# Performance work log

Hardware: AMD Instinct MI355X
Metric: run time of the kernel (lower is better)

The kernel has to match this reference:

```python
import jax, jax.numpy as jnp
import numpy as np

N_HEAD = 16
LORA_SCALE = 1.0 / 4.0  # alpha=1, r=4
LN_EPS = 1e-5


def _ln(x, g, b):
    # LayerNorm subclass casts to float32 then back to input dtype
    xf = x.astype(jnp.float32)
    m = xf.mean(-1, keepdims=True)
    v = xf.var(-1, keepdims=True)
    y = (xf - m) / jnp.sqrt(v + LN_EPS) * g + b
    return y.astype(x.dtype)


def _lora(h, a, b):
    # x @ a.T @ b.T * scaling ; a:[r,d], b:[d,r]
    return (h @ a.T) @ b.T * LORA_SCALE


def _attn(h, Wq, bq, Wk, Wv, bv, Wo, bo, la_k, lb_k, la_v, lb_v, la_o, lb_o):
    B, S, D = h.shape
    hd = D // N_HEAD
    scale = hd ** (-0.25)
    q = h @ Wq.T + bq
    k = h @ Wk.T + _lora(h, la_k, lb_k)          # key Linear has no bias
    v = h @ Wv.T + bv + _lora(h, la_v, lb_v)
    qh = q.reshape(B, S, N_HEAD, hd).transpose(0, 2, 1, 3) * scale  # [B,H,S,hd]
    kh = k.reshape(B, S, N_HEAD, hd).transpose(0, 2, 1, 3) * scale
    vh = v.reshape(B, S, N_HEAD, hd).transpose(0, 2, 1, 3)
    qk = jnp.einsum('bhqd,bhkd->bhqk', qh, kh).astype(jnp.float32)
    w = jax.nn.softmax(qk, axis=-1).astype(q.dtype)
    wv = jnp.einsum('bhqk,bhkd->bhqd', w, vh)
    wv = wv.transpose(0, 2, 1, 3).reshape(B, S, D)
    return wv @ Wo.T + bo + _lora(wv, la_o, lb_o)


def setup_inputs() -> dict:
    key = jax.random.key(0)
    D, R = 1024, 4
    B, S = 8, 1024
    ks = jax.random.split(key, 20)
    sd = 0.02
    inp = {
        'x': jax.random.normal(ks[0], (B, S, D), jnp.float32),
        'Wq': jax.random.normal(ks[1], (D, D), jnp.float32) * sd,
        'bq': jnp.zeros((D,), jnp.float32),
        'Wk': jax.random.normal(ks[2], (D, D), jnp.float32) * sd,
        'Wv': jax.random.normal(ks[3], (D, D), jnp.float32) * sd,
        'bv': jnp.zeros((D,), jnp.float32),
        'Wo': jax.random.normal(ks[4], (D, D), jnp.float32) * sd,
        'bo': jnp.zeros((D,), jnp.float32),
        'la_k': jax.random.normal(ks[5], (R, D), jnp.float32) * sd,
        'lb_k': jax.random.normal(ks[6], (D, R), jnp.float32) * sd,
        'la_v': jax.random.normal(ks[7], (R, D), jnp.float32) * sd,
        'lb_v': jax.random.normal(ks[8], (D, R), jnp.float32) * sd,
        'la_o': jax.random.normal(ks[9], (R, D), jnp.float32) * sd,
        'lb_o': jax.random.normal(ks[10], (D, R), jnp.float32) * sd,
        'g_attn': jnp.ones((D,), jnp.float32),
        'b_attn': jnp.zeros((D,), jnp.float32),
        'W1': jax.random.normal(ks[11], (4 * D, D), jnp.float32) * sd,
        'b1': jnp.zeros((4 * D,), jnp.float32),
        'W2': jax.random.normal(ks[12], (D, 4 * D), jnp.float32) * sd,
        'b2': jnp.zeros((D,), jnp.float32),
        'g_mlp': jnp.ones((D,), jnp.float32),
        'b_mlp': jnp.zeros((D,), jnp.float32),
    }
    return inp


def reference(x, Wq, bq, Wk, Wv, bv, Wo, bo, la_k, lb_k, la_v, lb_v, la_o, lb_o,
              g_attn, b_attn, W1, b1, W2, b2, g_mlp, b_mlp):
    # self-attention + residual (LoRA on key/value/out)
    x = x + _attn(_ln(x, g_attn, b_attn), Wq, bq, Wk, Wv, bv, Wo, bo,
                  la_k, lb_k, la_v, lb_v, la_o, lb_o)
    # MLP + residual (exact GELU, matching nn.GELU default)
    h = _ln(x, g_mlp, b_mlp)
    h = jax.nn.gelu(h @ W1.T + b1, approximate=False)
    x = x + h @ W2.T + b2
    return x
```

## Files before the change

kernel.cpp:

```cpp
#include <hip/hip_runtime.h>
#include <math.h>

typedef _Float16 f16_t;
typedef f16_t f16x8 __attribute__((ext_vector_type(8)));
typedef f16_t f16x4 __attribute__((ext_vector_type(4)));
typedef float f32x4 __attribute__((ext_vector_type(4)));
typedef float fv4 __attribute__((ext_vector_type(4)));

#define MFMA16(a, b, c) __builtin_amdgcn_mfma_f32_16x16x32_f16(a, b, c, 0, 0, 0)

__device__ __forceinline__ void gload16(const void* g, void* l) {
  __builtin_amdgcn_global_load_lds((const __attribute__((address_space(1))) void*)g,
                                   (__attribute__((address_space(3))) void*)l, 16, 0, 0);
}

__global__ __launch_bounds__(256) void ln_f32(const float* __restrict__ x,
                                              const float* __restrict__ g,
                                              const float* __restrict__ b,
                                              f16_t* __restrict__ y) {
  const int D = 1024;
  int row = blockIdx.x;
  int t = threadIdx.x;
  const float* xr = x + (size_t)row * D + t * 4;
  float x0 = xr[0], x1 = xr[1], x2 = xr[2], x3 = xr[3];
  float sum = x0 + x1 + x2 + x3;
  float sq = x0 * x0 + x1 * x1 + x2 * x2 + x3 * x3;
  for (int d = 32; d; d >>= 1) {
    sum += __shfl_down(sum, d);
    sq += __shfl_down(sq, d);
  }
  __shared__ float ssum[4], ssq[4];
  int w = t >> 6, lane = t & 63;
  if (lane == 0) { ssum[w] = sum; ssq[w] = sq; }
  __syncthreads();
  float ts = ssum[0] + ssum[1] + ssum[2] + ssum[3];
  float tq = ssq[0] + ssq[1] + ssq[2] + ssq[3];
  float mean = ts * (1.0f / 1024.0f);
  float var = tq * (1.0f / 1024.0f) - mean * mean;
  float rstd = rsqrtf(var + 1e-5f);
  f16_t* yr = y + (size_t)row * D + t * 4;
  const float* gr = g + t * 4;
  const float* br = b + t * 4;
  yr[0] = (f16_t)((x0 - mean) * rstd * gr[0] + br[0]);
  yr[1] = (f16_t)((x1 - mean) * rstd * gr[1] + br[1]);
  yr[2] = (f16_t)((x2 - mean) * rstd * gr[2] + br[2]);
  yr[3] = (f16_t)((x3 - mean) * rstd * gr[3] + br[3]);
}

__global__ __launch_bounds__(256) void ln_f16(const f16_t* __restrict__ x,
                                              const float* __restrict__ g,
                                              const float* __restrict__ b,
                                              f16_t* __restrict__ y) {
  const int D = 1024;
  int row = blockIdx.x;
  int t = threadIdx.x;
  const f16_t* xr = x + (size_t)row * D + t * 4;
  float x0 = (float)xr[0], x1 = (float)xr[1], x2 = (float)xr[2], x3 = (float)xr[3];
  float sum = x0 + x1 + x2 + x3;
  float sq = x0 * x0 + x1 * x1 + x2 * x2 + x3 * x3;
  for (int d = 32; d; d >>= 1) {
    sum += __shfl_down(sum, d);
    sq += __shfl_down(sq, d);
  }
  __shared__ float ssum[4], ssq[4];
  int w = t >> 6, lane = t & 63;
  if (lane == 0) { ssum[w] = sum; ssq[w] = sq; }
  __syncthreads();
  float ts = ssum[0] + ssum[1] + ssum[2] + ssum[3];
  float tq = ssq[0] + ssq[1] + ssq[2] + ssq[3];
  float mean = ts * (1.0f / 1024.0f);
  float var = tq * (1.0f / 1024.0f) - mean * mean;
  float rstd = rsqrtf(var + 1e-5f);
  f16_t* yr = y + (size_t)row * D + t * 4;
  const float* gr = g + t * 4;
  const float* br = b + t * 4;
  yr[0] = (f16_t)((x0 - mean) * rstd * gr[0] + br[0]);
  yr[1] = (f16_t)((x1 - mean) * rstd * gr[1] + br[1]);
  yr[2] = (f16_t)((x2 - mean) * rstd * gr[2] + br[2]);
  yr[3] = (f16_t)((x3 - mean) * rstd * gr[3] + br[3]);
}

__global__ __launch_bounds__(256) void convert_w(
    const float* __restrict__ wq, const float* __restrict__ wk,
    const float* __restrict__ wv, const float* __restrict__ wo,
    const float* __restrict__ w1, const float* __restrict__ w2,
    f16_t* __restrict__ oq, f16_t* __restrict__ ok, f16_t* __restrict__ ov,
    f16_t* __restrict__ oo, f16_t* __restrict__ o1, f16_t* __restrict__ o2) {
  int bid = blockIdx.x;
  const float* src;
  f16_t* dst;
  int bi;
  if (bid < 2048) {
    int seg = bid >> 9;
    bi = bid & 511;
    src = seg == 0 ? wq : seg == 1 ? wk : seg == 2 ? wv : wo;
    dst = seg == 0 ? oq : seg == 1 ? ok : seg == 2 ? ov : oo;
  } else if (bid < 4096) {
    bi = bid - 2048; src = w1; dst = o1;
  } else {
    bi = bid - 4096; src = w2; dst = o2;
  }
  size_t idx = (size_t)bi * 2048 + (size_t)threadIdx.x * 8;
  fv4 a = *(const fv4*)(src + idx);
  fv4 b = *(const fv4*)(src + idx + 4);
  f16x8 h;
#pragma unroll
  for (int j = 0; j < 4; ++j) { h[j] = (f16_t)a[j]; h[4 + j] = (f16_t)b[j]; }
  *(f16x8*)(dst + idx) = h;
}

__global__ __launch_bounds__(256) void lora_t_kernel(const f16_t* __restrict__ h,
                                                     const float* __restrict__ la,
                                                     float* __restrict__ t, int K) {
  int lane = threadIdx.x & 63;
  int w = threadIdx.x >> 6;
  int row = blockIdx.x * 4 + w;
  const f16_t* hrow = h + (size_t)row * K;
  float acc[4] = {0.f, 0.f, 0.f, 0.f};
  for (int it = 0; it < K / 512; ++it) {
    int base = it * 512 + lane * 8;
    f16x8 hx = *(const f16x8*)(hrow + base);
#pragma unroll
    for (int r = 0; r < 4; ++r) {
      const float* ar = la + (size_t)r * K + base;
#pragma unroll
      for (int j = 0; j < 8; ++j) acc[r] += (float)hx[j] * ar[j];
    }
  }
#pragma unroll
  for (int r = 0; r < 4; ++r) {
    for (int d = 32; d; d >>= 1) acc[r] += __shfl_down(acc[r], d);
  }
  if (lane == 0) {
#pragma unroll
    for (int r = 0; r < 4; ++r) t[(size_t)row * 4 + r] = acc[r];
  }
}

__global__ __launch_bounds__(256, 2) void gemm_f16(
    const f16_t* __restrict__ A, const f16_t* __restrict__ B,
    const float* __restrict__ bias, const float* __restrict__ loraT,
    const float* __restrict__ loraB, const float* residf,
    const f16_t* __restrict__ residb, f16_t* Cb, float* Cf, f16_t* Cvt,
    int M, int N, int K, int ldb, int dogelu) {
  __shared__ __align__(16) f16_t smem[2][16384];
  const int tid = threadIdx.x;
  const int lane = tid & 63, wid = tid >> 6;
  const int wm = wid >> 1, wn = wid & 1;
  const int l15 = lane & 15, lhi = lane >> 4;
  int nwg = gridDim.x * gridDim.y;
  int bid = blockIdx.y * gridDim.x + blockIdx.x;
  int swz = (bid & 7) * (nwg >> 3) + (bid >> 3);
  const int m0 = (swz / gridDim.x) * 128, n0 = (swz % gridDim.x) * 128;
  const int arow = tid >> 3;
  const int aslot = tid & 7;

  f32x4 acc[4][4];
#pragma unroll
  for (int i = 0; i < 4; ++i)
#pragma unroll
    for (int j = 0; j < 4; ++j) acc[i][j] = (f32x4){0.f, 0.f, 0.f, 0.f};

  auto stage = [&](const f16_t* G, int r0, int ldg, int step, char* lds) {
#pragma unroll
    for (int c = 0; c < 4; ++c) {
      int r = c * 32 + arow;
      int cm = aslot ^ (r & 7);
      gload16(G + (size_t)(r0 + r) * ldg + (size_t)step * 64 + cm * 8,
              lds + c * 4096 + wid * 1024);
    }
  };

  const int nsteps = K >> 6;
  stage(A, m0, K, 0, (char*)&smem[0][0]);
  stage(B, n0, ldb, 0, (char*)&smem[0][8192]);
  __syncthreads();
  for (int t = 0; t < nsteps; ++t) {
    int cur = t & 1, nxt = cur ^ 1;
    if (t + 1 < nsteps) {
      stage(A, m0, K, t + 1, (char*)&smem[nxt][0]);
      stage(B, n0, ldb, t + 1, (char*)&smem[nxt][8192]);
    }
    const char* As = (const char*)&smem[cur][0];
    const char* Bs = (const char*)&smem[cur][8192];
#pragma unroll
    for (int kk = 0; kk < 2; ++kk) {
      f16x8 af[4], bf[4];
#pragma unroll
      for (int i = 0; i < 4; ++i) {
        int row = wm * 64 + i * 16 + l15;
        af[i] = *(const f16x8*)(As + row * 128 + ((kk * 64 + lhi * 16) ^ ((row & 7) << 4)));
      }
#pragma unroll
      for (int j = 0; j < 4; ++j) {
        int row = wn * 64 + j * 16 + l15;
        bf[j] = *(const f16x8*)(Bs + row * 128 + ((kk * 64 + lhi * 16) ^ ((row & 7) << 4)));
      }
#pragma unroll
      for (int i = 0; i < 4; ++i)
#pragma unroll
        for (int j = 0; j < 4; ++j) acc[i][j] = MFMA16(af[i], bf[j], acc[i][j]);
    }
    __syncthreads();
  }

  const int gm = m0 + wm * 64, gn = n0 + wn * 64;
#pragma unroll
  for (int j = 0; j < 4; ++j) {
    int gcol = gn + j * 16 + l15;
    float bj = bias ? bias[gcol] : 0.f;
    float lb0 = 0.f, lb1 = 0.f, lb2 = 0.f, lb3 = 0.f;
    if (loraB) {
      const float* p = loraB + (size_t)gcol * 4;
      lb0 = p[0]; lb1 = p[1]; lb2 = p[2]; lb3 = p[3];
    }
#pragma unroll
    for (int i = 0; i < 4; ++i) {
      float v4[4];
#pragma unroll
      for (int r = 0; r < 4; ++r) {
        int grow = gm + i * 16 + lhi * 4 + r;
        float val = acc[i][j][r] + bj;
        if (loraT) {
          const float* tp = loraT + (size_t)grow * 4;
          val += 0.25f * (tp[0] * lb0 + tp[1] * lb1 + tp[2] * lb2 + tp[3] * lb3);
        }
        if (dogelu) val = 0.5f * val * (1.0f + erff(val * 0.70710678118654752f));
        if (residf) val += residf[(size_t)grow * N + gcol];
        if (residb) val += (float)residb[(size_t)grow * N + gcol];
        v4[r] = val;
      }
      if (Cf) {
#pragma unroll
        for (int r = 0; r < 4; ++r)
          Cf[(size_t)(gm + i * 16 + lhi * 4 + r) * N + gcol] = v4[r];
      } else if (Cvt) {
        int grow0 = gm + i * 16 + lhi * 4;
        int bb = grow0 >> 10, ss = grow0 & 1023;
        int hh = gcol >> 6, dd = gcol & 63;
        f16x4 pk;
#pragma unroll
        for (int r = 0; r < 4; ++r) pk[r] = (f16_t)v4[r];
        *(f16x4*)(Cvt + (((size_t)bb * 16 + hh) * 64 + dd) * 1024 + ss) = pk;
      } else {
#pragma unroll
        for (int r = 0; r < 4; ++r)
          Cb[(size_t)(gm + i * 16 + lhi * 4 + r) * N + gcol] = (f16_t)v4[r];
      }
    }
  }
}

__global__ __launch_bounds__(256, 2) void gemm_mfma(
    const f16_t* __restrict__ A, const float* __restrict__ B,
    const float* __restrict__ bias, const float* __restrict__ loraT,
    const float* __restrict__ loraB, const float* residf,
    const f16_t* __restrict__ residb, f16_t* Cb, float* Cf, f16_t* Cvt,
    int M, int N, int K, int ldb, int dogelu) {
  __shared__ __align__(16) f16_t smem[2][16384];
  const int tid = threadIdx.x;
  const int lane = tid & 63, wid = tid >> 6;
  const int wm = wid >> 1, wn = wid & 1;
  const int l15 = lane & 15, lhi = lane >> 4;
  const int m0 = blockIdx.y * 128, n0 = blockIdx.x * 128;
  const int arow = tid >> 3;
  const int aslot = tid & 7;

  f32x4 acc[4][4];
#pragma unroll
  for (int i = 0; i < 4; ++i)
#pragma unroll
    for (int j = 0; j < 4; ++j) acc[i][j] = (f32x4){0.f, 0.f, 0.f, 0.f};

  fv4 breg[4][2];

  auto stageA = [&](int step, int buf) {
#pragma unroll
    for (int c = 0; c < 4; ++c) {
      int r = c * 32 + arow;
      int cm = aslot ^ (r & 7);
      gload16(A + (size_t)(m0 + r) * K + (size_t)step * 64 + cm * 8,
              (char*)&smem[buf][0] + c * 4096 + wid * 1024);
    }
  };
  auto loadB = [&](int step) {
#pragma unroll
    for (int c = 0; c < 4; ++c) {
      int r = c * 32 + arow;
      const float* gp = B + (size_t)(n0 + r) * ldb + (size_t)step * 64 + aslot * 8;
      breg[c][0] = *(const fv4*)gp;
      breg[c][1] = *(const fv4*)(gp + 4);
    }
  };
  auto writeB = [&](int buf) {
#pragma unroll
    for (int c = 0; c < 4; ++c) {
      int r = c * 32 + arow;
      f16x8 hh;
#pragma unroll
      for (int j = 0; j < 4; ++j) hh[j] = (f16_t)breg[c][0][j];
#pragma unroll
      for (int j = 0; j < 4; ++j) hh[4 + j] = (f16_t)breg[c][1][j];
      int boff = r * 128 + ((aslot * 16) ^ ((r & 7) << 4));
      *(f16x8*)((char*)&smem[buf][8192] + boff) = hh;
    }
  };

  const int nsteps = K >> 6;
  stageA(0, 0);
  loadB(0);
  writeB(0);
  __syncthreads();
  for (int t = 0; t < nsteps; ++t) {
    int cur = t & 1, nxt = cur ^ 1;
    if (t + 1 < nsteps) { stageA(t + 1, nxt); loadB(t + 1); }
    const char* As = (const char*)&smem[cur][0];
    const char* Bs = (const char*)&smem[cur][8192];
#pragma unroll
    for (int kk = 0; kk < 2; ++kk) {
      f16x8 af[4], bf[4];
#pragma unroll
      for (int i = 0; i < 4; ++i) {
        int row = wm * 64 + i * 16 + l15;
        af[i] = *(const f16x8*)(As + row * 128 + ((kk * 64 + lhi * 16) ^ ((row & 7) << 4)));
      }
#pragma unroll
      for (int j = 0; j < 4; ++j) {
        int row = wn * 64 + j * 16 + l15;
        bf[j] = *(const f16x8*)(Bs + row * 128 + ((kk * 64 + lhi * 16) ^ ((row & 7) << 4)));
      }
#pragma unroll
      for (int i = 0; i < 4; ++i)
#pragma unroll
        for (int j = 0; j < 4; ++j) acc[i][j] = MFMA16(af[i], bf[j], acc[i][j]);
    }
    if (t + 1 < nsteps) writeB(nxt);
    __syncthreads();
  }

  const int gm = m0 + wm * 64, gn = n0 + wn * 64;
#pragma unroll
  for (int j = 0; j < 4; ++j) {
    int gcol = gn + j * 16 + l15;
    float bj = bias ? bias[gcol] : 0.f;
    float lb0 = 0.f, lb1 = 0.f, lb2 = 0.f, lb3 = 0.f;
    if (loraB) {
      const float* p = loraB + (size_t)gcol * 4;
      lb0 = p[0]; lb1 = p[1]; lb2 = p[2]; lb3 = p[3];
    }
#pragma unroll
    for (int i = 0; i < 4; ++i) {
      float v4[4];
#pragma unroll
      for (int r = 0; r < 4; ++r) {
        int grow = gm + i * 16 + lhi * 4 + r;
        float val = acc[i][j][r] + bj;
        if (loraT) {
          const float* tp = loraT + (size_t)grow * 4;
          val += 0.25f * (tp[0] * lb0 + tp[1] * lb1 + tp[2] * lb2 + tp[3] * lb3);
        }
        if (dogelu) val = 0.5f * val * (1.0f + erff(val * 0.70710678118654752f));
        if (residf) val += residf[(size_t)grow * N + gcol];
        if (residb) val += (float)residb[(size_t)grow * N + gcol];
        v4[r] = val;
      }
      if (Cf) {
#pragma unroll
        for (int r = 0; r < 4; ++r)
          Cf[(size_t)(gm + i * 16 + lhi * 4 + r) * N + gcol] = v4[r];
      } else if (Cvt) {
        int grow0 = gm + i * 16 + lhi * 4;
        int bb = grow0 >> 10, ss = grow0 & 1023;
        int hh = gcol >> 6, dd = gcol & 63;
        f16x4 pk;
#pragma unroll
        for (int r = 0; r < 4; ++r) pk[r] = (f16_t)v4[r];
        *(f16x4*)(Cvt + (((size_t)bb * 16 + hh) * 64 + dd) * 1024 + ss) = pk;
      } else {
#pragma unroll
        for (int r = 0; r < 4; ++r)
          Cb[(size_t)(gm + i * 16 + lhi * 4 + r) * N + gcol] = (f16_t)v4[r];
      }
    }
  }
}

__global__ __launch_bounds__(256, 3) void attn_mfma(const f16_t* __restrict__ q,
                                                    const f16_t* __restrict__ k,
                                                    const f16_t* __restrict__ vt,
                                                    f16_t* __restrict__ wv) {
  const int S = 1024, D = 1024;
  __shared__ __align__(16) f16_t Qs[128 * 64];
  __shared__ __align__(16) f16_t SP[128 * 64];
  __shared__ __align__(16) f16_t Ks[64 * 64];
  __shared__ __align__(16) f16_t Vts[64 * 64];
  __shared__ float rsb[128];
  __shared__ float lib[128];
  const int tid = threadIdx.x, lane = tid & 63, w = tid >> 6;
  const int l15 = lane & 15, lhi = lane >> 4;
  const int q0 = blockIdx.x * 128;
  const int h = blockIdx.y, b = blockIdx.z;
  const f16_t* qg = q + ((size_t)b * S + q0) * D + h * 64;
  const f16_t* kg = k + (size_t)b * S * D + h * 64;
  const f16_t* vg = vt + ((size_t)b * 16 + h) * 64 * (size_t)S;

#pragma unroll
  for (int c = 0; c < 4; ++c) {
    int r = c * 32 + (tid >> 3), kc = tid & 7;
    f16x8 xx = *(const f16x8*)(qg + (size_t)r * D + kc * 8);
    *(f16x8*)((char*)Qs + r * 128 + ((kc * 16) ^ ((r & 7) << 4))) = xx;
  }
  __syncthreads();
  f16x8 qf[2][2];
#pragma unroll
  for (int i = 0; i < 2; ++i) {
    int row = w * 32 + i * 16 + l15;
#pragma unroll
    for (int kk = 0; kk < 2; ++kk)
      qf[i][kk] = *(const f16x8*)((char*)Qs + row * 128 +
                                  ((kk * 64 + lhi * 16) ^ ((row & 7) << 4)));
  }

  f32x4 oacc[2][4];
#pragma unroll
  for (int i = 0; i < 2; ++i)
#pragma unroll
    for (int j = 0; j < 4; ++j) oacc[i][j] = (f32x4){0.f, 0.f, 0.f, 0.f};
  float m_run = -1e30f, l_run = 0.f;
  const int myrow = w * 32 + (lane >> 1);
  const int half = lane & 1;

  for (int kv = 0; kv < 16; ++kv) {
    __syncthreads();
#pragma unroll
    for (int c = 0; c < 2; ++c) {
      int r = c * 32 + (tid >> 3), kc = tid & 7;
      f16x8 xk = *(const f16x8*)(kg + (size_t)(kv * 64 + r) * D + kc * 8);
      *(f16x8*)((char*)Ks + r * 128 + ((kc * 16) ^ ((r & 7) << 4))) = xk;
      f16x8 xv = *(const f16x8*)(vg + (size_t)r * S + kv * 64 + kc * 8);
      *(f16x8*)((char*)Vts + r * 128 + ((kc * 16) ^ ((r & 7) << 4))) = xv;
    }
    __syncthreads();
    f32x4 sacc[2][4];
#pragma unroll
    for (int i = 0; i < 2; ++i)
#pragma unroll
      for (int j = 0; j < 4; ++j) sacc[i][j] = (f32x4){0.f, 0.f, 0.f, 0.f};
#pragma unroll
    for (int kk = 0; kk < 2; ++kk) {
      f16x8 kf[4];
#pragma unroll
      for (int j = 0; j < 4; ++j) {
        int row = j * 16 + l15;
        kf[j] = *(const f16x8*)((char*)Ks + row * 128 +
                                ((kk * 64 + lhi * 16) ^ ((row & 7) << 4)));
      }
#pragma unroll
      for (int i = 0; i < 2; ++i)
#pragma unroll
        for (int j = 0; j < 4; ++j) sacc[i][j] = MFMA16(qf[i][kk], kf[j], sacc[i][j]);
    }
#pragma unroll
    for (int i = 0; i < 2; ++i)
#pragma unroll
      for (int j = 0; j < 4; ++j)
#pragma unroll
        for (int r = 0; r < 4; ++r) {
          int srow = w * 32 + i * 16 + lhi * 4 + r;
          int scol = j * 16 + l15;
          *(f16_t*)((char*)SP + srow * 128 + ((scol * 2) ^ ((srow & 7) << 4))) =
              (f16_t)(sacc[i][j][r] * 0.125f);
        }
    __syncthreads();
    f16x8 ch[4];
#pragma unroll
    for (int c = 0; c < 4; ++c)
      ch[c] = *(const f16x8*)((char*)SP + myrow * 128 +
                              ((half * 64 + c * 16) ^ ((myrow & 7) << 4)));
    float mt = -1e30f;
#pragma unroll
    for (int c = 0; c < 4; ++c)
#pragma unroll
      for (int e = 0; e < 8; ++e) mt = fmaxf(mt, (float)ch[c][e]);
    mt = fmaxf(mt, __shfl_xor(mt, 1));
    float mnew = fmaxf(m_run, mt);
    float resc = __expf(m_run - mnew);
    float lsum = 0.f;
#pragma unroll
    for (int c = 0; c < 4; ++c) {
      f16x8 p8;
#pragma unroll
      for (int e = 0; e < 8; ++e) {
        float p = __expf((float)ch[c][e] - mnew);
        lsum += p;
        p8[e] = (f16_t)p;
      }
      *(f16x8*)((char*)SP + myrow * 128 + ((half * 64 + c * 16) ^ ((myrow & 7) << 4))) = p8;
    }
    lsum += __shfl_xor(lsum, 1);
    l_run = l_run * resc + lsum;
    m_run = mnew;
    if (half == 0) rsb[myrow] = resc;
    __syncthreads();
#pragma unroll
    for (int i = 0; i < 2; ++i) {
      float f0 = rsb[w * 32 + i * 16 + lhi * 4 + 0];
      float f1 = rsb[w * 32 + i * 16 + lhi * 4 + 1];
      float f2 = rsb[w * 32 + i * 16 + lhi * 4 + 2];
      float f3 = rsb[w * 32 + i * 16 + lhi * 4 + 3];
#pragma unroll
      for (int j = 0; j < 4; ++j) {
        oacc[i][j][0] *= f0;
        oacc[i][j][1] *= f1;
        oacc[i][j][2] *= f2;
        oacc[i][j][3] *= f3;
      }
    }
#pragma unroll
    for (int kk = 0; kk < 2; ++kk) {
      f16x8 pa[2], vb[4];
#pragma unroll
      for (int i = 0; i < 2; ++i) {
        int row = w * 32 + i * 16 + l15;
        pa[i] = *(const f16x8*)((char*)SP + row * 128 +
                                ((kk * 64 + lhi * 16) ^ ((row & 7) << 4)));
      }
#pragma unroll
      for (int j = 0; j < 4; ++j) {
        int row = j * 16 + l15;
        vb[j] = *(const f16x8*)((char*)Vts + row * 128 +
                                ((kk * 64 + lhi * 16) ^ ((row & 7) << 4)));
      }
#pragma unroll
      for (int i = 0; i < 2; ++i)
#pragma unroll
        for (int j = 0; j < 4; ++j) oacc[i][j] = MFMA16(pa[i], vb[j], oacc[i][j]);
    }
  }
  if (half == 0) lib[myrow] = 1.f / l_run;
  __syncthreads();
#pragma unroll
  for (int i = 0; i < 2; ++i)
#pragma unroll
    for (int r = 0; r < 4; ++r) {
      int row = w * 32 + i * 16 + lhi * 4 + r;
      float li = lib[row];
      size_t base = ((size_t)b * S + q0 + row) * D + h * 64;
#pragma unroll
      for (int j = 0; j < 4; ++j)
        wv[base + j * 16 + l15] = (f16_t)(oacc[i][j][r] * li);
    }
}

extern "C" void kernel_launch(void* const* d_in, const int* in_sizes, int n_in,
                              void* d_out, int out_size, void* d_ws, size_t ws_size,
                              hipStream_t stream) {
  const int B = 8, S = 1024, D = 1024, F = 4096;
  const int M = B * S;

  const float* x = (const float*)d_in[0];
  const float* Wq = (const float*)d_in[1];
  const float* bq = (const float*)d_in[2];
  const float* Wk = (const float*)d_in[3];
  const float* Wv = (const float*)d_in[4];
  const float* bv = (const float*)d_in[5];
  const float* Wo = (const float*)d_in[6];
  const float* bo = (const float*)d_in[7];
  const float* la_k = (const float*)d_in[8];
  const float* lb_k = (const float*)d_in[9];
  const float* la_v = (const float*)d_in[10];
  const float* lb_v = (const float*)d_in[11];
  const float* la_o = (const float*)d_in[12];
  const float* lb_o = (const float*)d_in[13];
  const float* g_attn = (const float*)d_in[14];
  const float* b_attn = (const float*)d_in[15];
  const float* W1 = (const float*)d_in[16];
  const float* b1 = (const float*)d_in[17];
  const float* W2 = (const float*)d_in[18];
  const float* b2 = (const float*)d_in[19];
  const float* g_mlp = (const float*)d_in[20];
  const float* b_mlp = (const float*)d_in[21];

  float* t_k = (float*)((char*)d_ws + 16);
  float* t_v = t_k + (size_t)M * 4;
  float* t_o = t_v + (size_t)M * 4;
  const size_t MD = (size_t)M * D;
  f16_t* P0 = (f16_t*)((char*)d_ws + 409600);
  f16_t* P1 = P0 + MD;
  f16_t* P2 = P0 + 2 * MD;
  f16_t* P3 = P0 + 3 * MD;
  f16_t* Wqf = P0 + 4 * MD;
  f16_t* Wkf = Wqf + (size_t)D * D;
  f16_t* Wvf = Wkf + (size_t)D * D;
  f16_t* Wof = Wvf + (size_t)D * D;
  f16_t* W1f = Wof + (size_t)D * D;
  f16_t* W2f = W1f + (size_t)F * D;
  float* outf = (float*)d_out;
  const size_t need = 409600 + 4 * MD * sizeof(f16_t) +
                      (4 * (size_t)D * D + 2 * (size_t)F * D) * sizeof(f16_t);
  const bool f16w = ws_size >= need;

  if (f16w)
    convert_w<<<6144, 256, 0, stream>>>(Wq, Wk, Wv, Wo, W1, W2,
                                        Wqf, Wkf, Wvf, Wof, W1f, W2f);

  ln_f32<<<M, 256, 0, stream>>>(x, g_attn, b_attn, P0);
  lora_t_kernel<<<M / 4, 256, 0, stream>>>(P0, la_k, t_k, D);
  lora_t_kernel<<<M / 4, 256, 0, stream>>>(P0, la_v, t_v, D);
  if (f16w) {
    gemm_f16<<<dim3(8, 64), 256, 0, stream>>>(
        P0, Wqf, bq, nullptr, nullptr, nullptr, nullptr, P1, nullptr, nullptr,
        M, D, D, D, 0);
    gemm_f16<<<dim3(8, 64), 256, 0, stream>>>(
        P0, Wkf, nullptr, t_k, lb_k, nullptr, nullptr, P2, nullptr, nullptr,
        M, D, D, D, 0);
    gemm_f16<<<dim3(8, 64), 256, 0, stream>>>(
        P0, Wvf, bv, t_v, lb_v, nullptr, nullptr, nullptr, nullptr, P3,
        M, D, D, D, 0);
  } else {
    gemm_mfma<<<dim3(8, 64), 256, 0, stream>>>(
        P0, Wq, bq, nullptr, nullptr, nullptr, nullptr, P1, nullptr, nullptr,
        M, D, D, D, 0);
    gemm_mfma<<<dim3(8, 64), 256, 0, stream>>>(
        P0, Wk, nullptr, t_k, lb_k, nullptr, nullptr, P2, nullptr, nullptr,
        M, D, D, D, 0);
    gemm_mfma<<<dim3(8, 64), 256, 0, stream>>>(
        P0, Wv, bv, t_v, lb_v, nullptr, nullptr, nullptr, nullptr, P3,
        M, D, D, D, 0);
  }
  attn_mfma<<<dim3(8, 16, 8), 256, 0, stream>>>(P1, P2, P3, P0);
  lora_t_kernel<<<M / 4, 256, 0, stream>>>(P0, la_o, t_o, D);
  if (f16w)
    gemm_f16<<<dim3(8, 64), 256, 0, stream>>>(
        P0, Wof, bo, t_o, lb_o, x, nullptr, P3, nullptr, nullptr, M, D, D, D, 0);
  else
    gemm_mfma<<<dim3(8, 64), 256, 0, stream>>>(
        P0, Wo, bo, t_o, lb_o, x, nullptr, P3, nullptr, nullptr, M, D, D, D, 0);
  ln_f16<<<M, 256, 0, stream>>>(P3, g_mlp, b_mlp, P0);
  if (f16w) {
    gemm_f16<<<dim3(16, 64), 256, 0, stream>>>(
        P0, W1f, b1, nullptr, nullptr, nullptr, nullptr, P1, nullptr, nullptr,
        M, 2048, D, D, 1);
    gemm_f16<<<dim3(8, 64), 256, 0, stream>>>(
        P1, W2f, b2, nullptr, nullptr, nullptr, P3, nullptr, outf, nullptr,
        M, D, 2048, F, 0);
    gemm_f16<<<dim3(16, 64), 256, 0, stream>>>(
        P0, W1f + (size_t)2048 * D, b1 + 2048, nullptr, nullptr, nullptr, nullptr,
        P1, nullptr, nullptr, M, 2048, D, D, 1);
    gemm_f16<<<dim3(8, 64), 256, 0, stream>>>(
        P1, W2f + 2048, nullptr, nullptr, nullptr, outf, nullptr, nullptr, outf,
        nullptr, M, D, 2048, F, 0);
  } else {
    gemm_mfma<<<dim3(16, 64), 256, 0, stream>>>(
        P0, W1, b1, nullptr, nullptr, nullptr, nullptr, P1, nullptr, nullptr,
        M, 2048, D, D, 1);
    gemm_mfma<<<dim3(8, 64), 256, 0, stream>>>(
        P1, W2, b2, nullptr, nullptr, nullptr, P3, nullptr, outf, nullptr,
        M, D, 2048, F, 0);
    gemm_mfma<<<dim3(16, 64), 256, 0, stream>>>(
        P0, W1 + (size_t)2048 * D, b1 + 2048, nullptr, nullptr, nullptr, nullptr,
        P1, nullptr, nullptr, M, 2048, D, D, 1);
    gemm_mfma<<<dim3(8, 64), 256, 0, stream>>>(
        P1, W2 + 2048, nullptr, nullptr, nullptr, outf, nullptr, nullptr, outf,
        nullptr, M, D, 2048, F, 0);
  }
}
```

Measured before the change: 662.5 us.

## Fuse QKV projections into one GEMM and merge K/V LoRA kernels

Stores the Wq/Wk/Wv f16 copies contiguously so a single gemm_qkv launch over a 3072-wide N covers all three projections, with a per-segment epilogue for bias, LoRA and the transposed V layout. The two LoRA-A reductions for K and V become one kernel that reads the LN output once. Both GEMMs drop LDS double buffering for a single buffer and raise the occupancy hint to 3 blocks per CU, trading load/compute overlap within a block for more resident blocks to hide latency.

```diff
diff --git a/kernel.cpp b/kernel.cpp
--- a/kernel.cpp
+++ b/kernel.cpp
@@ -109,6 +109,47 @@
   *(f16x8*)(dst + idx) = h;
 }
 
+__global__ __launch_bounds__(256) void lora_kv_kernel(
+    const f16_t* __restrict__ h, const float* __restrict__ la_k,
+    const float* __restrict__ la_v, float* __restrict__ t_k,
+    float* __restrict__ t_v, int K) {
+  int lane = threadIdx.x & 63;
+  int w = threadIdx.x >> 6;
+  int row = blockIdx.x * 4 + w;
+  const f16_t* hrow = h + (size_t)row * K;
+  float ak[4] = {0.f, 0.f, 0.f, 0.f};
+  float av[4] = {0.f, 0.f, 0.f, 0.f};
+  for (int it = 0; it < K / 512; ++it) {
+    int base = it * 512 + lane * 8;
+    f16x8 hx = *(const f16x8*)(hrow + base);
+#pragma unroll
+    for (int r = 0; r < 4; ++r) {
+      const float* kr = la_k + (size_t)r * K + base;
+      const float* vr = la_v + (size_t)r * K + base;
+#pragma unroll
+      for (int j = 0; j < 8; ++j) {
+        float hv = (float)hx[j];
+        ak[r] += hv * kr[j];
+        av[r] += hv * vr[j];
+      }
+    }
+  }
+#pragma unroll
+  for (int r = 0; r < 4; ++r) {
+    for (int d = 32; d; d >>= 1) {
+      ak[r] += __shfl_down(ak[r], d);
+      av[r] += __shfl_down(av[r], d);
+    }
+  }
+  if (lane == 0) {
+#pragma unroll
+    for (int r = 0; r < 4; ++r) {
+      t_k[(size_t)row * 4 + r] = ak[r];
+      t_v[(size_t)row * 4 + r] = av[r];
+    }
+  }
+}
+
 __global__ __launch_bounds__(256) void lora_t_kernel(const f16_t* __restrict__ h,
                                                      const float* __restrict__ la,
                                                      float* __restrict__ t, int K) {
@@ -137,13 +178,123 @@
   }
 }
 
-__global__ __launch_bounds__(256, 2) void gemm_f16(
+__global__ __launch_bounds__(256, 3) void gemm_qkv(
+    const f16_t* __restrict__ A, const f16_t* __restrict__ W,
+    const float* __restrict__ bq, const float* __restrict__ bv,
+    const float* __restrict__ t_k, const float* __restrict__ lb_k,
+    const float* __restrict__ t_v, const float* __restrict__ lb_v,
+    f16_t* __restrict__ Pq, f16_t* __restrict__ Pk, f16_t* __restrict__ Pvt,
+    int K) {
+  const int D = 1024;
+  __shared__ __align__(16) f16_t Asm[8192];
+  __shared__ __align__(16) f16_t Bsm[8192];
+  const int tid = threadIdx.x;
+  const int lane = tid & 63, wid = tid >> 6;
+  const int wm = wid >> 1, wn = wid & 1;
+  const int l15 = lane & 15, lhi = lane >> 4;
+  int nwg = gridDim.x * gridDim.y;
+  int bid = blockIdx.y * gridDim.x + blockIdx.x;
+  int swz = (bid & 7) * (nwg >> 3) + (bid >> 3);
+  const int m0 = (swz / gridDim.x) * 128, n0 = (swz % gridDim.x) * 128;
+  const int seg = n0 >> 10;
+  const int arow = tid >> 3;
+  const int aslot = tid & 7;
+
+  f32x4 acc[4][4];
+#pragma unroll
+  for (int i = 0; i < 4; ++i)
+#pragma unroll
+    for (int j = 0; j < 4; ++j) acc[i][j] = (f32x4){0.f, 0.f, 0.f, 0.f};
+
+  auto stage = [&](const f16_t* G, int r0, int ldg, int step, char* lds) {
+#pragma unroll
+    for (int c = 0; c < 4; ++c) {
+      int r = c * 32 + arow;
+      int cm = aslot ^ (r & 7);
+      gload16(G + (size_t)(r0 + r) * ldg + (size_t)step * 64 + cm * 8,
+              lds + c * 4096 + wid * 1024);
+    }
+  };
+
+  const int nsteps = K >> 6;
+  for (int t = 0; t < nsteps; ++t) {
+    if (t) __syncthreads();
+    stage(A, m0, K, t, (char*)Asm);
+    stage(W, n0, K, t, (char*)Bsm);
+    __syncthreads();
+#pragma unroll
+    for (int kk = 0; kk < 2; ++kk) {
+      f16x8 af[4], bf[4];
+#pragma unroll
+      for (int i = 0; i < 4; ++i) {
+        int row = wm * 64 + i * 16 + l15;
+        af[i] = *(const f16x8*)((char*)Asm + row * 128 +
+                                ((kk * 64 + lhi * 16) ^ ((row & 7) << 4)));
+      }
+#pragma unroll
+      for (int j = 0; j < 4; ++j) {
+        int row = wn * 64 + j * 16 + l15;
+        bf[j] = *(const f16x8*)((char*)Bsm + row * 128 +
+                                ((kk * 64 + lhi * 16) ^ ((row & 7) << 4)));
+      }
+#pragma unroll
+      for (int i = 0; i < 4; ++i)
+#pragma unroll
+        for (int j = 0; j < 4; ++j) acc[i][j] = MFMA16(af[i], bf[j], acc[i][j]);
+    }
+  }
+
+  const int gm = m0 + wm * 64, gn = n0 + wn * 64;
+  const float* tB = (seg == 1) ? t_k : t_v;
+#pragma unroll
+  for (int j = 0; j < 4; ++j) {
+    int gcol = gn + j * 16 + l15;
+    int c = gcol & 1023;
+    float bj = (seg == 0) ? bq[c] : (seg == 2 ? bv[c] : 0.f);
+    float lb0 = 0.f, lb1 = 0.f, lb2 = 0.f, lb3 = 0.f;
+    if (seg) {
+      const float* p = (seg == 1 ? lb_k : lb_v) + (size_t)c * 4;
+      lb0 = p[0]; lb1 = p[1]; lb2 = p[2]; lb3 = p[3];
+    }
+#pragma unroll
+    for (int i = 0; i < 4; ++i) {
+      float v4[4];
+#pragma unroll
+      for (int r = 0; r < 4; ++r) {
+        int grow = gm + i * 16 + lhi * 4 + r;
+        float val = acc[i][j][r] + bj;
+        if (seg) {
+          const float* tp = tB + (size_t)grow * 4;
+          val += 0.25f * (tp[0] * lb0 + tp[1] * lb1 + tp[2] * lb2 + tp[3] * lb3);
+        }
+        v4[r] = val;
+      }
+      if (seg < 2) {
+        f16_t* dst = (seg == 0) ? Pq : Pk;
+#pragma unroll
+        for (int r = 0; r < 4; ++r)
+          dst[(size_t)(gm + i * 16 + lhi * 4 + r) * D + c] = (f16_t)v4[r];
+      } else {
+        int grow0 = gm + i * 16 + lhi * 4;
+        int bb = grow0 >> 10, ss = grow0 & 1023;
+        int hh = c >> 6, dd = c & 63;
+        f16x4 pk;
+#pragma unroll
+        for (int r = 0; r < 4; ++r) pk[r] = (f16_t)v4[r];
+        *(f16x4*)(Pvt + (((size_t)bb * 16 + hh) * 64 + dd) * 1024 + ss) = pk;
+      }
+    }
+  }
+}
+
+__global__ __launch_bounds__(256, 3) void gemm_f16(
     const f16_t* __restrict__ A, const f16_t* __restrict__ B,
     const float* __restrict__ bias, const float* __restrict__ loraT,
     const float* __restrict__ loraB, const float* residf,
-    const f16_t* __restrict__ residb, f16_t* Cb, float* Cf, f16_t* Cvt,
+    const f16_t* __restrict__ residb, f16_t* Cb, float* Cf,
     int M, int N, int K, int ldb, int dogelu) {
-  __shared__ __align__(16) f16_t smem[2][16384];
+  __shared__ __align__(16) f16_t Asm[8192];
+  __shared__ __align__(16) f16_t Bsm[8192];
   const int tid = threadIdx.x;
   const int lane = tid & 63, wid = tid >> 6;
   const int wm = wid >> 1, wn = wid & 1;
@@ -172,36 +323,31 @@
   };
 
   const int nsteps = K >> 6;
-  stage(A, m0, K, 0, (char*)&smem[0][0]);
-  stage(B, n0, ldb, 0, (char*)&smem[0][8192]);
-  __syncthreads();
   for (int t = 0; t < nsteps; ++t) {
-    int cur = t & 1, nxt = cur ^ 1;
-    if (t + 1 < nsteps) {
-      stage(A, m0, K, t + 1, (char*)&smem[nxt][0]);
-      stage(B, n0, ldb, t + 1, (char*)&smem[nxt][8192]);
-    }
-    const char* As = (const char*)&smem[cur][0];
-    const char* Bs = (const char*)&smem[cur][8192];
+    if (t) __syncthreads();
+    stage(A, m0, K, t, (char*)Asm);
+    stage(B, n0, ldb, t, (char*)Bsm);
+    __syncthreads();
 #pragma unroll
     for (int kk = 0; kk < 2; ++kk) {
       f16x8 af[4], bf[4];
 #pragma unroll
       for (int i = 0; i < 4; ++i) {
         int row = wm * 64 + i * 16 + l15;
-        af[i] = *(const f16x8*)(As + row * 128 + ((kk * 64 + lhi * 16) ^ ((row & 7) << 4)));
+        af[i] = *(const f16x8*)((char*)Asm + row * 128 +
+                                ((kk * 64 + lhi * 16) ^ ((row & 7) << 4)));
       }
 #pragma unroll
       for (int j = 0; j < 4; ++j) {
         int row = wn * 64 + j * 16 + l15;
-        bf[j] = *(const f16x8*)(Bs + row * 128 + ((kk * 64 + lhi * 16) ^ ((row & 7) << 4)));
+        bf[j] = *(const f16x8*)((char*)Bsm + row * 128 +
+                                ((kk * 64 + lhi * 16) ^ ((row & 7) << 4)));
       }
 #pragma unroll
       for (int i = 0; i < 4; ++i)
 #pragma unroll
         for (int j = 0; j < 4; ++j) acc[i][j] = MFMA16(af[i], bf[j], acc[i][j]);
     }
-    __syncthreads();
   }
 
   const int gm = m0 + wm * 64, gn = n0 + wn * 64;
@@ -234,14 +380,6 @@
 #pragma unroll
         for (int r = 0; r < 4; ++r)
           Cf[(size_t)(gm + i * 16 + lhi * 4 + r) * N + gcol] = v4[r];
-      } else if (Cvt) {
-        int grow0 = gm + i * 16 + lhi * 4;
-        int bb = grow0 >> 10, ss = grow0 & 1023;
-        int hh = gcol >> 6, dd = gcol & 63;
-        f16x4 pk;
-#pragma unroll
-        for (int r = 0; r < 4; ++r) pk[r] = (f16_t)v4[r];
-        *(f16x4*)(Cvt + (((size_t)bb * 16 + hh) * 64 + dd) * 1024 + ss) = pk;
       } else {
 #pragma unroll
         for (int r = 0; r < 4; ++r)
@@ -589,10 +727,8 @@
   f16_t* P1 = P0 + MD;
   f16_t* P2 = P0 + 2 * MD;
   f16_t* P3 = P0 + 3 * MD;
-  f16_t* Wqf = P0 + 4 * MD;
-  f16_t* Wkf = Wqf + (size_t)D * D;
-  f16_t* Wvf = Wkf + (size_t)D * D;
-  f16_t* Wof = Wvf + (size_t)D * D;
+  f16_t* Wqkvf = P0 + 4 * MD;
+  f16_t* Wof = Wqkvf + 3 * (size_t)D * D;
   f16_t* W1f = Wof + (size_t)D * D;
   f16_t* W2f = W1f + (size_t)F * D;
   float* outf = (float*)d_out;
@@ -601,22 +737,15 @@
   const bool f16w = ws_size >= need;
 
   if (f16w)
-    convert_w<<<6144, 256, 0, stream>>>(Wq, Wk, Wv, Wo, W1, W2,
-                                        Wqf, Wkf, Wvf, Wof, W1f, W2f);
+    convert_w<<<6144, 256, 0, stream>>>(
+        Wq, Wk, Wv, Wo, W1, W2, Wqkvf, Wqkvf + (size_t)D * D,
+        Wqkvf + 2 * (size_t)D * D, Wof, W1f, W2f);
 
   ln_f32<<<M, 256, 0, stream>>>(x, g_attn, b_attn, P0);
-  lora_t_kernel<<<M / 4, 256, 0, stream>>>(P0, la_k, t_k, D);
-  lora_t_kernel<<<M / 4, 256, 0, stream>>>(P0, la_v, t_v, D);
+  lora_kv_kernel<<<M / 4, 256, 0, stream>>>(P0, la_k, la_v, t_k, t_v, D);
   if (f16w) {
-    gemm_f16<<<dim3(8, 64), 256, 0, stream>>>(
-        P0, Wqf, bq, nullptr, nullptr, nullptr, nullptr, P1, nullptr, nullptr,
-        M, D, D, D, 0);
-    gemm_f16<<<dim3(8, 64), 256, 0, stream>>>(
-        P0, Wkf, nullptr, t_k, lb_k, nullptr, nullptr, P2, nullptr, nullptr,
-        M, D, D, D, 0);
-    gemm_f16<<<dim3(8, 64), 256, 0, stream>>>(
-        P0, Wvf, bv, t_v, lb_v, nullptr, nullptr, nullptr, nullptr, P3,
-        M, D, D, D, 0);
+    gemm_qkv<<<dim3(24, 64), 256, 0, stream>>>(
+        P0, Wqkvf, bq, bv, t_k, lb_k, t_v, lb_v, P1, P2, P3, D);
   } else {
     gemm_mfma<<<dim3(8, 64), 256, 0, stream>>>(
         P0, Wq, bq, nullptr, nullptr, nullptr, nullptr, P1, nullptr, nullptr,
@@ -632,24 +761,24 @@
   lora_t_kernel<<<M / 4, 256, 0, stream>>>(P0, la_o, t_o, D);
   if (f16w)
     gemm_f16<<<dim3(8, 64), 256, 0, stream>>>(
-        P0, Wof, bo, t_o, lb_o, x, nullptr, P3, nullptr, nullptr, M, D, D, D, 0);
+        P0, Wof, bo, t_o, lb_o, x, nullptr, P3, nullptr, M, D, D, D, 0);
   else
     gemm_mfma<<<dim3(8, 64), 256, 0, stream>>>(
         P0, Wo, bo, t_o, lb_o, x, nullptr, P3, nullptr, nullptr, M, D, D, D, 0);
   ln_f16<<<M, 256, 0, stream>>>(P3, g_mlp, b_mlp, P0);
   if (f16w) {
     gemm_f16<<<dim3(16, 64), 256, 0, stream>>>(
-        P0, W1f, b1, nullptr, nullptr, nullptr, nullptr, P1, nullptr, nullptr,
+        P0, W1f, b1, nullptr, nullptr, nullptr, nullptr, P1, nullptr,
         M, 2048, D, D, 1);
     gemm_f16<<<dim3(8, 64), 256, 0, stream>>>(
-        P1, W2f, b2, nullptr, nullptr, nullptr, P3, nullptr, outf, nullptr,
+        P1, W2f, b2, nullptr, nullptr, nullptr, P3, nullptr, outf,
         M, D, 2048, F, 0);
     gemm_f16<<<dim3(16, 64), 256, 0, stream>>>(
         P0, W1f + (size_t)2048 * D, b1 + 2048, nullptr, nullptr, nullptr, nullptr,
-        P1, nullptr, nullptr, M, 2048, D, D, 1);
+        P1, nullptr, M, 2048, D, D, 1);
     gemm_f16<<<dim3(8, 64), 256, 0, stream>>>(
         P1, W2f + 2048, nullptr, nullptr, nullptr, outf, nullptr, nullptr, outf,
-        nullptr, M, D, 2048, F, 0);
+        M, D, 2048, F, 0);
   } else {
     gemm_mfma<<<dim3(16, 64), 256, 0, stream>>>(
         P0, W1, b1, nullptr, nullptr, nullptr, nullptr, P1, nullptr, nullptr,
```

New measurement: 663.3 us. No clear change (+0.1%).
